# Performance work log

Hardware: AMD Instinct MI355X
Metric: run time of the kernel (lower is better)

The kernel has to match this reference:

```python
import jax, jax.numpy as jnp
import numpy as np

EMBED = 768
HIDDEN = 4 * EMBED
TEMPERATURE = 1.0
LN_EPS = 1e-5


def setup_inputs() -> dict:
    key = jax.random.key(0)
    ks = jax.random.split(key, 10)
    s = 1.0 / np.sqrt(EMBED)
    sh = 1.0 / np.sqrt(HIDDEN)
    return {
        "x": jax.random.normal(ks[0], (32, 577, EMBED), dtype=jnp.float32),
        "Wq": jax.random.normal(ks[1], (EMBED, EMBED), dtype=jnp.float32) * s,
        "Wk": jax.random.normal(ks[2], (EMBED, EMBED), dtype=jnp.float32) * s,
        "Wv": jax.random.normal(ks[3], (EMBED, EMBED), dtype=jnp.float32) * s,
        "ln1_g": jnp.ones((EMBED,), jnp.float32),
        "ln1_b": jnp.zeros((EMBED,), jnp.float32),
        "ln2_g": jnp.ones((EMBED,), jnp.float32),
        "ln2_b": jnp.zeros((EMBED,), jnp.float32),
        "W1": jax.random.normal(ks[4], (EMBED, HIDDEN), dtype=jnp.float32) * s,
        "b1": jnp.zeros((HIDDEN,), jnp.float32),
        "W2": jax.random.normal(ks[5], (HIDDEN, EMBED), dtype=jnp.float32) * sh,
        "b2": jnp.zeros((EMBED,), jnp.float32),
    }


def layer_norm(x, g, b):
    mu = jnp.mean(x, axis=-1, keepdims=True)
    var = jnp.mean(jnp.square(x - mu), axis=-1, keepdims=True)
    return (x - mu) * jax.lax.rsqrt(var + LN_EPS) * g + b


def l2_attention(h, Wq, Wk, Wv):
    # h: [b, s, d]
    Q = h @ Wq
    K = h @ Wk
    V = h @ Wv
    q_sq = jnp.sum(Q * Q, axis=-1, keepdims=True)          # [b, s, 1]
    k_sq = jnp.sum(K * K, axis=-1, keepdims=True)          # [b, s, 1]
    qk = jnp.einsum('bqd,bkd->bqk', Q, K)                  # [b, s, s]
    l2_sq = q_sq + jnp.swapaxes(k_sq, -2, -1) - 2.0 * qk
    attn = jax.nn.softmax(-l2_sq / TEMPERATURE, axis=-1)
    return jnp.einsum('bqk,bkd->bqd', attn, V)


def reference(x, Wq, Wk, Wv, ln1_g, ln1_b, ln2_g, ln2_b, W1, b1, W2, b2):
    x = x + l2_attention(layer_norm(x, ln1_g, ln1_b), Wq, Wk, Wv)
    h = layer_norm(x, ln2_g, ln2_b)
    h = jax.nn.gelu(h @ W1 + b1, approximate=False) @ W2 + b2
    return x + h
```

## Files before the change

kernel.cpp:

```cpp
#include <hip/hip_runtime.h>

#define EMBED 768
#define HIDDEN 3072
#define SEQ 577
#define BATCH 32
#define ROWS (BATCH*SEQ)
#define KPAD 608
#define SLD 640

typedef __attribute__((ext_vector_type(4))) float f32x4;
typedef __attribute__((ext_vector_type(8))) __bf16 bf16x8;
typedef unsigned int __attribute__((address_space(1))) as1_u32;
typedef unsigned int __attribute__((address_space(3))) as3_u32;

__device__ __forceinline__ unsigned short f2b(float f) {
    unsigned int u = __float_as_uint(f);
    u = u + 0x7FFFu + ((u >> 16) & 1u);
    return (unsigned short)(u >> 16);
}
__device__ __forceinline__ float b2f(unsigned short s) {
    return __uint_as_float(((unsigned int)s) << 16);
}
__device__ __forceinline__ void gld16(const unsigned short* g, unsigned short* l) {
    __builtin_amdgcn_global_load_lds((const as1_u32*)g, (as3_u32*)l, 16, 0, 0);
}
__device__ __forceinline__ float gelu_f(float x) {
    float u = x * (0.7978845608028654f + 0.03567740814183f * x * x);
    float e = __expf(2.0f * u);
    float th = 1.0f - 2.0f / (e + 1.0f);
    return 0.5f * x * (1.0f + th);
}

__device__ __forceinline__ int swz_lin() {
    int nx = gridDim.x;
    int lin = blockIdx.y * nx + blockIdx.x;
    if (gridDim.z == 1) {
        int nwg = nx * gridDim.y;
        int q = nwg >> 3, r = nwg & 7;
        int xcd = lin & 7, blk = lin >> 3;
        lin = (xcd < r ? xcd * (q + 1) : r * (q + 1) + (xcd - r) * q) + blk;
    }
    return lin;
}

__global__ void ln_kernel(const float* __restrict__ x, const float* __restrict__ g,
                          const float* __restrict__ b, unsigned short* __restrict__ o) {
    int row = blockIdx.x;
    const float* xr = x + (size_t)row * EMBED;
    int t = threadIdx.x;
    float v0 = xr[t], v1 = xr[t + 256], v2 = xr[t + 512];
    float s = v0 + v1 + v2;
    float ss = v0 * v0 + v1 * v1 + v2 * v2;
#pragma unroll
    for (int d = 32; d; d >>= 1) { s += __shfl_down(s, d); ss += __shfl_down(ss, d); }
    __shared__ float rs[4], rss[4];
    if ((t & 63) == 0) { rs[t >> 6] = s; rss[t >> 6] = ss; }
    __syncthreads();
    s = rs[0] + rs[1] + rs[2] + rs[3];
    ss = rss[0] + rss[1] + rss[2] + rss[3];
    float mu = s * (1.0f / EMBED);
    float var = ss * (1.0f / EMBED) - mu * mu;
    float rstd = rsqrtf(var + 1e-5f);
    unsigned short* orow = o + (size_t)row * EMBED;
    orow[t]       = f2b((v0 - mu) * rstd * g[t]       + b[t]);
    orow[t + 256] = f2b((v1 - mu) * rstd * g[t + 256] + b[t + 256]);
    orow[t + 512] = f2b((v2 - mu) * rstd * g[t + 512] + b[t + 512]);
}

__global__ void ln_split_kernel(const float* __restrict__ x, const float* __restrict__ g,
                                const float* __restrict__ b, unsigned short* __restrict__ oh,
                                unsigned short* __restrict__ ol) {
    int row = blockIdx.x;
    const float* xr = x + (size_t)row * EMBED;
    int t = threadIdx.x;
    float v0 = xr[t], v1 = xr[t + 256], v2 = xr[t + 512];
    float s = v0 + v1 + v2;
    float ss = v0 * v0 + v1 * v1 + v2 * v2;
#pragma unroll
    for (int d = 32; d; d >>= 1) { s += __shfl_down(s, d); ss += __shfl_down(ss, d); }
    __shared__ float rs[4], rss[4];
    if ((t & 63) == 0) { rs[t >> 6] = s; rss[t >> 6] = ss; }
    __syncthreads();
    s = rs[0] + rs[1] + rs[2] + rs[3];
    ss = rss[0] + rss[1] + rss[2] + rss[3];
    float mu = s * (1.0f / EMBED);
    float var = ss * (1.0f / EMBED) - mu * mu;
    float rstd = rsqrtf(var + 1e-5f);
    size_t base = (size_t)row * EMBED;
#pragma unroll
    for (int i = 0; i < 3; i++) {
        int d = t + 256 * i;
        float v = (i == 0 ? v0 : (i == 1 ? v1 : v2));
        float y = (v - mu) * rstd * g[d] + b[d];
        unsigned short h = f2b(y);
        oh[base + d] = h;
        ol[base + d] = f2b(y - b2f(h));
    }
}

__global__ void ksq_kernel(const unsigned short* __restrict__ qh,
                           const unsigned short* __restrict__ ql, float* __restrict__ ksq) {
    int row = blockIdx.x;
    int t = threadIdx.x;
    size_t base = (size_t)row * 1536 + EMBED;
    float s = 0.f;
#pragma unroll
    for (int i = 0; i < 3; i++) {
        int d = t + 256 * i;
        float k = b2f(qh[base + d]) + b2f(ql[base + d]);
        s += k * k;
    }
#pragma unroll
    for (int d = 32; d; d >>= 1) s += __shfl_down(s, d);
    __shared__ float rs[4];
    if ((t & 63) == 0) rs[t >> 6] = s;
    __syncthreads();
    if (t == 0) ksq[row] = rs[0] + rs[1] + rs[2] + rs[3];
}

__global__ void softmax_kernel(const float* __restrict__ S, unsigned short* __restrict__ P) {
    int r = blockIdx.x;
    int t = threadIdx.x;
    const float* sr = S + (size_t)r * SLD;
    float v0 = sr[t];
    float v1 = sr[t + 256];
    float v2 = (t + 512 < SEQ) ? sr[t + 512] : -3.0e38f;
    float m = fmaxf(v0, fmaxf(v1, v2));
#pragma unroll
    for (int d = 32; d; d >>= 1) m = fmaxf(m, __shfl_down(m, d));
    __shared__ float rm[4];
    if ((t & 63) == 0) rm[t >> 6] = m;
    __syncthreads();
    m = fmaxf(fmaxf(rm[0], rm[1]), fmaxf(rm[2], rm[3]));
    float e0 = __expf(v0 - m);
    float e1 = __expf(v1 - m);
    float e2 = (t + 512 < SEQ) ? __expf(v2 - m) : 0.0f;
    float s = e0 + e1 + e2;
#pragma unroll
    for (int d = 32; d; d >>= 1) s += __shfl_down(s, d);
    __shared__ float rsum[4];
    if ((t & 63) == 0) rsum[t >> 6] = s;
    __syncthreads();
    float inv = 1.0f / (rsum[0] + rsum[1] + rsum[2] + rsum[3]);
    unsigned short* pr = P + (size_t)r * KPAD;
    pr[t]       = f2b(e0 * inv);
    pr[t + 256] = f2b(e1 * inv);
    if (t + 512 < KPAD) pr[t + 512] = f2b(e2 * inv);
}

__global__ void wt_kernel(const float* __restrict__ in, unsigned short* __restrict__ out,
                          int K, int N, int outRowOff, int outLd) {
    __shared__ float tile[32][33];
    int n0 = blockIdx.x * 32, k0 = blockIdx.y * 32;
    int tx = threadIdx.x, ty = threadIdx.y;
#pragma unroll
    for (int i = 0; i < 4; i++)
        tile[ty + 8 * i][tx] = in[(size_t)(k0 + ty + 8 * i) * N + (n0 + tx)];
    __syncthreads();
#pragma unroll
    for (int i = 0; i < 4; i++)
        out[(size_t)(outRowOff + n0 + ty + 8 * i) * outLd + (k0 + tx)] = f2b(tile[tx][ty + 8 * i]);
}

__global__ void wt_split2_kernel(const float* __restrict__ Wq, const float* __restrict__ Wk,
                                 unsigned short* __restrict__ oh, unsigned short* __restrict__ ol) {
    const float* in = blockIdx.z ? Wk : Wq;
    int outRowOff = blockIdx.z * EMBED;
    __shared__ float tile[32][33];
    int n0 = blockIdx.x * 32, k0 = blockIdx.y * 32;
    int tx = threadIdx.x, ty = threadIdx.y;
#pragma unroll
    for (int i = 0; i < 4; i++)
        tile[ty + 8 * i][tx] = in[(size_t)(k0 + ty + 8 * i) * EMBED + (n0 + tx)];
    __syncthreads();
#pragma unroll
    for (int i = 0; i < 4; i++) {
        float v = tile[tx][ty + 8 * i];
        unsigned short h = f2b(v);
        size_t idx = (size_t)(outRowOff + n0 + ty + 8 * i) * EMBED + (k0 + tx);
        oh[idx] = h;
        ol[idx] = f2b(v - b2f(h));
    }
}

template <int EPI>
__global__ __launch_bounds__(256, 2) void gemm_bt128(
    const unsigned short* __restrict__ A, int lda, long long sA,
    const unsigned short* __restrict__ B, int ldb, long long sB,
    int M, int N, int K,
    void* __restrict__ C, int ldc, long long sC,
    const float* __restrict__ E, long long sE) {
    __shared__ unsigned short As[2][4096];
    __shared__ unsigned short Bs[2][4096];
    int z = blockIdx.z;
    A += (size_t)z * sA;
    B += (size_t)z * sB;
    int nx = gridDim.x;
    int lin = swz_lin();
    int row0 = (lin / nx) * 128, col0 = (lin % nx) * 128;
    int t = threadIdx.x, l = t & 63, w = t >> 6;
    int wr = w >> 1, wc = w & 1;
    int l15 = l & 15, kb = l >> 4;

    f32x4 acc[4][4] = {};

    int srow = t >> 2;
    int kboff = ((t & 3) ^ ((srow >> 1) & 3)) * 8;

    int aoE[2], boE[2];
#pragma unroll
    for (int c = 0; c < 2; ++c) {
        int ar = row0 + c * 64 + srow; ar = ar < M ? ar : M - 1;
        aoE[c] = ar * lda + kboff;
        int br = col0 + c * 64 + srow; br = br < N ? br : N - 1;
        boE[c] = br * ldb + kboff;
    }
    int aoff[4], boff[4];
#pragma unroll
    for (int m = 0; m < 4; m++) {
        int r = wr * 64 + m * 16 + l15;
        aoff[m] = r * 32 + (kb ^ ((r >> 1) & 3)) * 8;
        int rn = wc * 64 + m * 16 + l15;
        boff[m] = rn * 32 + (kb ^ ((rn >> 1) & 3)) * 8;
    }

    auto compute = [&](int sl) {
        bf16x8 af[4], bfr[4];
#pragma unroll
        for (int m = 0; m < 4; m++) af[m] = *reinterpret_cast<const bf16x8*>(&As[sl][aoff[m]]);
#pragma unroll
        for (int n = 0; n < 4; n++) bfr[n] = *reinterpret_cast<const bf16x8*>(&Bs[sl][boff[n]]);
#pragma unroll
        for (int m = 0; m < 4; m++)
#pragma unroll
            for (int n = 0; n < 4; n++)
                acc[m][n] = __builtin_amdgcn_mfma_f32_16x16x32_bf16(af[m], bfr[n], acc[m][n], 0, 0, 0);
    };

    int ldsoff = t * 8;
    for (int kt = 0; kt < K; kt += 64) {
        gld16(A + (size_t)(aoE[0] + kt), &As[0][ldsoff]);
        gld16(A + (size_t)(aoE[1] + kt), &As[0][2048 + ldsoff]);
        gld16(B + (size_t)(boE[0] + kt), &Bs[0][ldsoff]);
        gld16(B + (size_t)(boE[1] + kt), &Bs[0][2048 + ldsoff]);
        bool has2 = (kt + 32) < K;
        if (has2) {
            gld16(A + (size_t)(aoE[0] + kt + 32), &As[1][ldsoff]);
            gld16(A + (size_t)(aoE[1] + kt + 32), &As[1][2048 + ldsoff]);
            gld16(B + (size_t)(boE[0] + kt + 32), &Bs[1][ldsoff]);
            gld16(B + (size_t)(boE[1] + kt + 32), &Bs[1][2048 + ldsoff]);
        }
        asm volatile("s_waitcnt vmcnt(0)" ::: "memory");
        __builtin_amdgcn_s_barrier();
        __builtin_amdgcn_sched_barrier(0);
        compute(0);
        if (has2) compute(1);
        __builtin_amdgcn_s_barrier();
        __builtin_amdgcn_sched_barrier(0);
    }

    int rbase = row0 + wr * 64 + (l >> 4) * 4;
    int cbase = col0 + wc * 64 + l15;
    auto epi = [&](bool chk) {
#pragma unroll
        for (int m = 0; m < 4; m++) {
#pragma unroll
            for (int n = 0; n < 4; n++) {
                int col = cbase + n * 16;
                if (chk && col >= N) continue;
#pragma unroll
                for (int j = 0; j < 4; j++) {
                    int row = rbase + m * 16 + j;
                    if (chk && row >= M) continue;
                    float v = acc[m][n][j];
                    size_t oidx = (size_t)z * sC + (size_t)row * ldc + col;
                    if (EPI == 0) {
                        ((unsigned short*)C)[oidx] = f2b(v);
                    } else if (EPI == 3) {
                        ((unsigned short*)C)[oidx] = f2b(gelu_f(v + E[col]));
                    } else if (EPI == 4) {
                        ((float*)C)[oidx] += v + E[col];
                    }
                }
            }
        }
    };
    if (row0 + 128 <= M && col0 + 128 <= N) epi(false); else epi(true);
}

template <int EPI>
__global__ __launch_bounds__(512, 4) void gemm_bt256(
    const unsigned short* __restrict__ A, int lda, long long sA,
    const unsigned short* __restrict__ B, int ldb, long long sB,
    int M, int N, int K,
    void* __restrict__ C, int ldc, long long sC,
    const float* __restrict__ E, long long sE) {
    __shared__ unsigned short As[3][8192];
    __shared__ unsigned short Bs[3][4096];
    int z = blockIdx.z;
    A += (size_t)z * sA;
    B += (size_t)z * sB;
    int nx = gridDim.x;
    int lin = swz_lin();
    int row0 = (lin / nx) * 256, col0 = (lin % nx) * 128;
    int t = threadIdx.x, l = t & 63, w = t >> 6;
    int wr = w >> 1, wc = w & 1;
    int l15 = l & 15, kb = l >> 4;

    f32x4 acc[4][4] = {};

    int srow = t >> 2;
    int kboff = ((t & 3) ^ ((srow >> 1) & 3)) * 8;

    int aoE[2], boE;
#pragma unroll
    for (int c = 0; c < 2; ++c) {
        int ar = row0 + c * 128 + srow; ar = ar < M ? ar : M - 1;
        aoE[c] = ar * lda + kboff;
    }
    {
        int br = col0 + srow; br = br < N ? br : N - 1;
        boE = br * ldb + kboff;
    }
    int aoff[4], boff[4];
#pragma unroll
    for (int m = 0; m < 4; m++) {
        int r = wr * 64 + m * 16 + l15;
        aoff[m] = r * 32 + (kb ^ ((r >> 1) & 3)) * 8;
        int rn = wc * 64 + m * 16 + l15;
        boff[m] = rn * 32 + (kb ^ ((rn >> 1) & 3)) * 8;
    }

    auto compute = [&](int sl) {
        bf16x8 af[4], bfr[4];
#pragma unroll
        for (int m = 0; m < 4; m++) af[m] = *reinterpret_cast<const bf16x8*>(&As[sl][aoff[m]]);
#pragma unroll
        for (int n = 0; n < 4; n++) bfr[n] = *reinterpret_cast<const bf16x8*>(&Bs[sl][boff[n]]);
#pragma unroll
        for (int m = 0; m < 4; m++)
#pragma unroll
            for (int n = 0; n < 4; n++)
                acc[m][n] = __builtin_amdgcn_mfma_f32_16x16x32_bf16(af[m], bfr[n], acc[m][n], 0, 0, 0);
    };

    int ldsoff = t * 8;
    for (int kt = 0; kt < K; kt += 96) {
#pragma unroll
        for (int s = 0; s < 3; ++s) {
            int ks = kt + 32 * s;
            if (ks < K) {
                gld16(A + (size_t)(aoE[0] + ks), &As[s][ldsoff]);
                gld16(A + (size_t)(aoE[1] + ks), &As[s][4096 + ldsoff]);
                gld16(B + (size_t)(boE + ks), &Bs[s][ldsoff]);
            }
        }
        asm volatile("s_waitcnt vmcnt(0)" ::: "memory");
        __builtin_amdgcn_s_barrier();
        __builtin_amdgcn_sched_barrier(0);
#pragma unroll
        for (int s = 0; s < 3; ++s)
            if (kt + 32 * s < K) compute(s);
        __builtin_amdgcn_s_barrier();
        __builtin_amdgcn_sched_barrier(0);
    }

    int rbase = row0 + wr * 64 + (l >> 4) * 4;
    int cbase = col0 + wc * 64 + l15;
    auto epi = [&](bool chk) {
#pragma unroll
        for (int m = 0; m < 4; m++) {
#pragma unroll
            for (int n = 0; n < 4; n++) {
                int col = cbase + n * 16;
                if (chk && col >= N) continue;
#pragma unroll
                for (int j = 0; j < 4; j++) {
                    int row = rbase + m * 16 + j;
                    if (chk && row >= M) continue;
                    float v = acc[m][n][j];
                    if (EPI == 5) {
                        int zz = row / SEQ;
                        int cc = row - zz * SEQ;
                        ((unsigned short*)C)[(size_t)zz * (EMBED * KPAD) + (size_t)col * KPAD + cc] = f2b(v);
                    } else {
                        size_t oidx = (size_t)z * sC + (size_t)row * ldc + col;
                        if (EPI == 2) {
                            ((float*)C)[oidx] = E[oidx] + v;
                        } else if (EPI == 4) {
                            ((float*)C)[oidx] += v + E[col];
                        }
                    }
                }
            }
        }
    };
    if (row0 + 256 <= M && col0 + 128 <= N) epi(false); else epi(true);
}

template <int EPI>
__global__ __launch_bounds__(512, 2) void gemm_hp(
    const unsigned short* __restrict__ Ah, const unsigned short* __restrict__ Al, int lda, long long sA,
    const unsigned short* __restrict__ Bh, const unsigned short* __restrict__ Bl, int ldb, long long sB,
    int M, int N, int K,
    void* __restrict__ C, int ldc, long long sC, long long planeOff,
    const float* __restrict__ E, long long sE) {
    __shared__ unsigned short Ash[8192], Asl[8192], Bsh[4096], Bsl[4096];
    int z = blockIdx.z;
    Ah += (size_t)z * sA; Al += (size_t)z * sA;
    Bh += (size_t)z * sB; Bl += (size_t)z * sB;
    int nx = gridDim.x;
    int lin = swz_lin();
    int row0 = (lin / nx) * 256, col0 = (lin % nx) * 128;
    int t = threadIdx.x, l = t & 63, w = t >> 6;
    int wr = w >> 1, wc = w & 1;
    int l15 = l & 15, kb = l >> 4;

    f32x4 acc[4][4] = {};

    int srow = t >> 2;
    int kboff = ((t & 3) ^ ((srow >> 1) & 3)) * 8;

    int aoE[2], boE;
#pragma unroll
    for (int c = 0; c < 2; ++c) {
        int ar = row0 + c * 128 + srow; ar = ar < M ? ar : M - 1;
        aoE[c] = ar * lda + kboff;
    }
    {
        int br = col0 + srow; br = br < N ? br : N - 1;
        boE = br * ldb + kboff;
    }
    int aoff[4], boff[4];
#pragma unroll
    for (int m = 0; m < 4; m++) {
        int r = wr * 64 + m * 16 + l15;
        aoff[m] = r * 32 + (kb ^ ((r >> 1) & 3)) * 8;
        int rn = wc * 64 + m * 16 + l15;
        boff[m] = rn * 32 + (kb ^ ((rn >> 1) & 3)) * 8;
    }

    int ldsoff = t * 8;
    for (int kt = 0; kt < K; kt += 32) {
        gld16(Ah + (size_t)(aoE[0] + kt), &Ash[ldsoff]);
        gld16(Ah + (size_t)(aoE[1] + kt), &Ash[4096 + ldsoff]);
        gld16(Al + (size_t)(aoE[0] + kt), &Asl[ldsoff]);
        gld16(Al + (size_t)(aoE[1] + kt), &Asl[4096 + ldsoff]);
        gld16(Bh + (size_t)(boE + kt), &Bsh[ldsoff]);
        gld16(Bl + (size_t)(boE + kt), &Bsl[ldsoff]);
        __syncthreads();
        bf16x8 afh[4], afl[4], bfh[4], bfl[4];
#pragma unroll
        for (int m = 0; m < 4; m++) {
            afh[m] = *reinterpret_cast<const bf16x8*>(&Ash[aoff[m]]);
            afl[m] = *reinterpret_cast<const bf16x8*>(&Asl[aoff[m]]);
        }
#pragma unroll
        for (int n = 0; n < 4; n++) {
            bfh[n] = *reinterpret_cast<const bf16x8*>(&Bsh[boff[n]]);
            bfl[n] = *reinterpret_cast<const bf16x8*>(&Bsl[boff[n]]);
        }
#pragma unroll
        for (int m = 0; m < 4; m++)
#pragma unroll
            for (int n = 0; n < 4; n++) {
                acc[m][n] = __builtin_amdgcn_mfma_f32_16x16x32_bf16(afh[m], bfh[n], acc[m][n], 0, 0, 0);
                acc[m][n] = __builtin_amdgcn_mfma_f32_16x16x32_bf16(afh[m], bfl[n], acc[m][n], 0, 0, 0);
                acc[m][n] = __builtin_amdgcn_mfma_f32_16x16x32_bf16(afl[m], bfh[n], acc[m][n], 0, 0, 0);
            }
        __syncthreads();
    }

    int rbase = row0 + wr * 64 + (l >> 4) * 4;
    int cbase = col0 + wc * 64 + l15;
    auto epi = [&](bool chk) {
#pragma unroll
        for (int m = 0; m < 4; m++) {
#pragma unroll
            for (int n = 0; n < 4; n++) {
                int col = cbase + n * 16;
                if (chk && col >= N) continue;
#pragma unroll
                for (int j = 0; j < 4; j++) {
                    int row = rbase + m * 16 + j;
                    if (chk && row >= M) continue;
                    float v = acc[m][n][j];
                    size_t oidx = (size_t)z * sC + (size_t)row * ldc + col;
                    if (EPI == 0) {
                        unsigned short h = f2b(v);
                        ((unsigned short*)C)[oidx] = h;
                        ((unsigned short*)C)[oidx + planeOff] = f2b(v - b2f(h));
                    } else if (EPI == 1) {
                        ((float*)C)[oidx] = 2.0f * v - E[(size_t)z * sE + col];
                    }
                }
            }
        }
    };
    if (row0 + 256 <= M && col0 + 128 <= N) epi(false); else epi(true);
}

extern "C" void kernel_launch(void* const* d_in, const int* in_sizes, int n_in,
                              void* d_out, int out_size, void* d_ws, size_t ws_size,
                              hipStream_t stream) {
    const float* x   = (const float*)d_in[0];
    const float* Wq  = (const float*)d_in[1];
    const float* Wk  = (const float*)d_in[2];
    const float* Wv  = (const float*)d_in[3];
    const float* g1  = (const float*)d_in[4];
    const float* be1 = (const float*)d_in[5];
    const float* g2  = (const float*)d_in[6];
    const float* be2 = (const float*)d_in[7];
    const float* W1  = (const float*)d_in[8];
    const float* bb1 = (const float*)d_in[9];
    const float* W2  = (const float*)d_in[10];
    const float* bb2 = (const float*)d_in[11];
    float* out = (float*)d_out;

    char* ws = (char*)d_ws;
    size_t off = 0;
    auto alloc = [&](size_t bytes) -> char* {
        char* p = ws + off;
        off += (bytes + 255) & ~(size_t)255;
        return p;
    };
    unsigned short* wqkTh = (unsigned short*)alloc((size_t)1536 * EMBED * 2);
    unsigned short* wqkTl = (unsigned short*)alloc((size_t)1536 * EMBED * 2);
    unsigned short* wvT   = (unsigned short*)alloc((size_t)EMBED * EMBED * 2);
    unsigned short* w1T   = (unsigned short*)alloc((size_t)HIDDEN * EMBED * 2);
    unsigned short* w2T   = (unsigned short*)alloc((size_t)EMBED * HIDDEN * 2);
    float*          ksqb  = (float*)alloc((size_t)ROWS * 4);
    char* regB = alloc((size_t)ROWS * HIDDEN * 2);
    char* regC = alloc((size_t)2 * ROWS * EMBED * 2);
    unsigned short* vtb   = (unsigned short*)alloc((size_t)BATCH * EMBED * KPAD * 2);
    unsigned short* Pbuf  = (unsigned short*)alloc((size_t)ROWS * KPAD * 2);
    if (off > ws_size) return;

    unsigned short* qkh  = (unsigned short*)regB;
    unsigned short* qkl  = qkh + (size_t)ROWS * 1536;
    unsigned short* hid  = (unsigned short*)regB;
    unsigned short* h1h  = (unsigned short*)regC;
    unsigned short* h1l  = h1h + (size_t)ROWS * EMBED;
    float*          Sbuf = (float*)regC;
    unsigned short* h2   = (unsigned short*)regC;

    dim3 b256(256), b512(512), bT(32, 8);

    wt_split2_kernel<<<dim3(24, 24, 2), bT, 0, stream>>>(Wq, Wk, wqkTh, wqkTl);
    wt_kernel<<<dim3(24, 24), bT, 0, stream>>>(Wv, wvT, EMBED, EMBED, 0, EMBED);
    wt_kernel<<<dim3(96, 24), bT, 0, stream>>>(W1, w1T, EMBED, HIDDEN, 0, EMBED);
    wt_kernel<<<dim3(24, 96), bT, 0, stream>>>(W2, w2T, HIDDEN, EMBED, 0, HIDDEN);

    ln_split_kernel<<<ROWS, b256, 0, stream>>>(x, g1, be1, h1h, h1l);

    gemm_hp<0><<<dim3(12, 73, 1), b512, 0, stream>>>(
        h1h, h1l, EMBED, 0, wqkTh, wqkTl, EMBED, 0,
        ROWS, 1536, EMBED, qkh, 1536, 0, (long long)ROWS * 1536, nullptr, 0);

    gemm_bt256<5><<<dim3(6, 73, 1), b512, 0, stream>>>(
        h1h, EMBED, 0, wvT, EMBED, 0, ROWS, EMBED, EMBED, vtb, 0, 0, nullptr, 0);

    ksq_kernel<<<ROWS, b256, 0, stream>>>(qkh, qkl, ksqb);

    gemm_hp<1><<<dim3(5, 3, 32), b512, 0, stream>>>(
        qkh, qkl, 1536, (long long)SEQ * 1536, qkh + EMBED, qkl + EMBED, 1536, (long long)SEQ * 1536,
        SEQ, SEQ, EMBED, Sbuf, SLD, (long long)SEQ * SLD, 0, ksqb, SEQ);

    softmax_kernel<<<ROWS, b256, 0, stream>>>(Sbuf, Pbuf);

    gemm_bt256<2><<<dim3(6, 3, 32), b512, 0, stream>>>(
        Pbuf, KPAD, (long long)SEQ * KPAD, vtb, KPAD, (long long)EMBED * KPAD,
        SEQ, EMBED, KPAD, out, EMBED, (long long)SEQ * EMBED, x, (long long)SEQ * EMBED);

    ln_kernel<<<ROWS, b256, 0, stream>>>(out, g2, be2, h2);

    gemm_bt128<3><<<dim3(24, 145, 1), b256, 0, stream>>>(
        h2, EMBED, 0, w1T, EMBED, 0, ROWS, HIDDEN, EMBED, hid, HIDDEN, 0, bb1, 0);

    gemm_bt256<4><<<dim3(6, 73, 1), b512, 0, stream>>>(
        hid, HIDDEN, 0, w2T, HIDDEN, 0, ROWS, EMBED, HIDDEN, out, EMBED, 0, bb2, 0);
}
```

Before: 727.6 us.

## Fuse V projection into split-precision QK GEMM launch with per-tile single-pass mode

The separate bf16 GEMM that produced the transposed V buffer is removed. The QK split-precision GEMM launch is widened to cover Q, K and V columns using one concatenated transposed weight. Tiles whose columns fall in the V range skip the low-precision loads and extra MFMAs, and write bf16 transposed V directly. This saves a kernel launch and a pass over the LN output. In exchange, V now goes through the 256x128 hp tile path with a runtime branch inside the k-loop.

```diff
diff --git a/kernel.cpp b/kernel.cpp
--- a/kernel.cpp
+++ b/kernel.cpp
@@ -379,17 +379,11 @@
                     int row = rbase + m * 16 + j;
                     if (chk && row >= M) continue;
                     float v = acc[m][n][j];
-                    if (EPI == 5) {
-                        int zz = row / SEQ;
-                        int cc = row - zz * SEQ;
-                        ((unsigned short*)C)[(size_t)zz * (EMBED * KPAD) + (size_t)col * KPAD + cc] = f2b(v);
-                    } else {
-                        size_t oidx = (size_t)z * sC + (size_t)row * ldc + col;
-                        if (EPI == 2) {
-                            ((float*)C)[oidx] = E[oidx] + v;
-                        } else if (EPI == 4) {
-                            ((float*)C)[oidx] += v + E[col];
-                        }
+                    size_t oidx = (size_t)z * sC + (size_t)row * ldc + col;
+                    if (EPI == 2) {
+                        ((float*)C)[oidx] = E[oidx] + v;
+                    } else if (EPI == 4) {
+                        ((float*)C)[oidx] += v + E[col];
                     }
                 }
             }
@@ -404,7 +398,8 @@
     const unsigned short* __restrict__ Bh, const unsigned short* __restrict__ Bl, int ldb, long long sB,
     int M, int N, int K,
     void* __restrict__ C, int ldc, long long sC, long long planeOff,
-    const float* __restrict__ E, long long sE) {
+    const float* __restrict__ E, long long sE,
+    int vcol0, unsigned short* __restrict__ vt) {
     __shared__ unsigned short Ash[8192], Asl[8192], Bsh[4096], Bsl[4096];
     int z = blockIdx.z;
     Ah += (size_t)z * sA; Al += (size_t)z * sA;
@@ -412,6 +407,7 @@
     int nx = gridDim.x;
     int lin = swz_lin();
     int row0 = (lin / nx) * 256, col0 = (lin % nx) * 128;
+    bool vpass = (EPI == 0) && (col0 >= vcol0);
     int t = threadIdx.x, l = t & 63, w = t >> 6;
     int wr = w >> 1, wc = w & 1;
     int l15 = l & 15, kb = l >> 4;
@@ -444,30 +440,37 @@
     for (int kt = 0; kt < K; kt += 32) {
         gld16(Ah + (size_t)(aoE[0] + kt), &Ash[ldsoff]);
         gld16(Ah + (size_t)(aoE[1] + kt), &Ash[4096 + ldsoff]);
-        gld16(Al + (size_t)(aoE[0] + kt), &Asl[ldsoff]);
-        gld16(Al + (size_t)(aoE[1] + kt), &Asl[4096 + ldsoff]);
         gld16(Bh + (size_t)(boE + kt), &Bsh[ldsoff]);
-        gld16(Bl + (size_t)(boE + kt), &Bsl[ldsoff]);
+        if (!vpass) {
+            gld16(Al + (size_t)(aoE[0] + kt), &Asl[ldsoff]);
+            gld16(Al + (size_t)(aoE[1] + kt), &Asl[4096 + ldsoff]);
+            gld16(Bl + (size_t)(boE + kt), &Bsl[ldsoff]);
+        }
         __syncthreads();
-        bf16x8 afh[4], afl[4], bfh[4], bfl[4];
-#pragma unroll
-        for (int m = 0; m < 4; m++) {
-            afh[m] = *reinterpret_cast<const bf16x8*>(&Ash[aoff[m]]);
-            afl[m] = *reinterpret_cast<const bf16x8*>(&Asl[aoff[m]]);
-        }
-#pragma unroll
-        for (int n = 0; n < 4; n++) {
-            bfh[n] = *reinterpret_cast<const bf16x8*>(&Bsh[boff[n]]);
-            bfl[n] = *reinterpret_cast<const bf16x8*>(&Bsl[boff[n]]);
-        }
+        bf16x8 afh[4], bfh[4];
+#pragma unroll
+        for (int m = 0; m < 4; m++) afh[m] = *reinterpret_cast<const bf16x8*>(&Ash[aoff[m]]);
+#pragma unroll
+        for (int n = 0; n < 4; n++) bfh[n] = *reinterpret_cast<const bf16x8*>(&Bsh[boff[n]]);
 #pragma unroll
         for (int m = 0; m < 4; m++)
 #pragma unroll
-            for (int n = 0; n < 4; n++) {
+            for (int n = 0; n < 4; n++)
                 acc[m][n] = __builtin_amdgcn_mfma_f32_16x16x32_bf16(afh[m], bfh[n], acc[m][n], 0, 0, 0);
-                acc[m][n] = __builtin_amdgcn_mfma_f32_16x16x32_bf16(afh[m], bfl[n], acc[m][n], 0, 0, 0);
-                acc[m][n] = __builtin_amdgcn_mfma_f32_16x16x32_bf16(afl[m], bfh[n], acc[m][n], 0, 0, 0);
-            }
+        if (!vpass) {
+            bf16x8 afl[4], bfl[4];
+#pragma unroll
+            for (int m = 0; m < 4; m++) afl[m] = *reinterpret_cast<const bf16x8*>(&Asl[aoff[m]]);
+#pragma unroll
+            for (int n = 0; n < 4; n++) bfl[n] = *reinterpret_cast<const bf16x8*>(&Bsl[boff[n]]);
+#pragma unroll
+            for (int m = 0; m < 4; m++)
+#pragma unroll
+                for (int n = 0; n < 4; n++) {
+                    acc[m][n] = __builtin_amdgcn_mfma_f32_16x16x32_bf16(afh[m], bfl[n], acc[m][n], 0, 0, 0);
+                    acc[m][n] = __builtin_amdgcn_mfma_f32_16x16x32_bf16(afl[m], bfh[n], acc[m][n], 0, 0, 0);
+                }
+        }
         __syncthreads();
     }
 
@@ -485,13 +488,19 @@
                     int row = rbase + m * 16 + j;
                     if (chk && row >= M) continue;
                     float v = acc[m][n][j];
-                    size_t oidx = (size_t)z * sC + (size_t)row * ldc + col;
-                    if (EPI == 0) {
-                        unsigned short h = f2b(v);
-                        ((unsigned short*)C)[oidx] = h;
-                        ((unsigned short*)C)[oidx + planeOff] = f2b(v - b2f(h));
-                    } else if (EPI == 1) {
-                        ((float*)C)[oidx] = 2.0f * v - E[(size_t)z * sE + col];
+                    if (vpass) {
+                        int zz = row / SEQ;
+                        int cc = row - zz * SEQ;
+                        vt[(size_t)zz * (EMBED * KPAD) + (size_t)(col - vcol0) * KPAD + cc] = f2b(v);
+                    } else {
+                        size_t oidx = (size_t)z * sC + (size_t)row * ldc + col;
+                        if (EPI == 0) {
+                            unsigned short h = f2b(v);
+                            ((unsigned short*)C)[oidx] = h;
+                            ((unsigned short*)C)[oidx + planeOff] = f2b(v - b2f(h));
+                        } else if (EPI == 1) {
+                            ((float*)C)[oidx] = 2.0f * v - E[(size_t)z * sE + col];
+                        }
                     }
                 }
             }
@@ -524,9 +533,8 @@
         off += (bytes + 255) & ~(size_t)255;
         return p;
     };
-    unsigned short* wqkTh = (unsigned short*)alloc((size_t)1536 * EMBED * 2);
-    unsigned short* wqkTl = (unsigned short*)alloc((size_t)1536 * EMBED * 2);
-    unsigned short* wvT   = (unsigned short*)alloc((size_t)EMBED * EMBED * 2);
+    unsigned short* wqkvTh = (unsigned short*)alloc((size_t)2304 * EMBED * 2);
+    unsigned short* wqkvTl = (unsigned short*)alloc((size_t)2304 * EMBED * 2);
     unsigned short* w1T   = (unsigned short*)alloc((size_t)HIDDEN * EMBED * 2);
     unsigned short* w2T   = (unsigned short*)alloc((size_t)EMBED * HIDDEN * 2);
     float*          ksqb  = (float*)alloc((size_t)ROWS * 4);
@@ -546,25 +554,24 @@
 
     dim3 b256(256), b512(512), bT(32, 8);
 
-    wt_split2_kernel<<<dim3(24, 24, 2), bT, 0, stream>>>(Wq, Wk, wqkTh, wqkTl);
-    wt_kernel<<<dim3(24, 24), bT, 0, stream>>>(Wv, wvT, EMBED, EMBED, 0, EMBED);
+    wt_split2_kernel<<<dim3(24, 24, 2), bT, 0, stream>>>(Wq, Wk, wqkvTh, wqkvTl);
+    wt_kernel<<<dim3(24, 24), bT, 0, stream>>>(Wv, wqkvTh, EMBED, EMBED, 1536, EMBED);
     wt_kernel<<<dim3(96, 24), bT, 0, stream>>>(W1, w1T, EMBED, HIDDEN, 0, EMBED);
     wt_kernel<<<dim3(24, 96), bT, 0, stream>>>(W2, w2T, HIDDEN, EMBED, 0, HIDDEN);
 
     ln_split_kernel<<<ROWS, b256, 0, stream>>>(x, g1, be1, h1h, h1l);
 
-    gemm_hp<0><<<dim3(12, 73, 1), b512, 0, stream>>>(
-        h1h, h1l, EMBED, 0, wqkTh, wqkTl, EMBED, 0,
-        ROWS, 1536, EMBED, qkh, 1536, 0, (long long)ROWS * 1536, nullptr, 0);
-
-    gemm_bt256<5><<<dim3(6, 73, 1), b512, 0, stream>>>(
-        h1h, EMBED, 0, wvT, EMBED, 0, ROWS, EMBED, EMBED, vtb, 0, 0, nullptr, 0);
+    gemm_hp<0><<<dim3(18, 73, 1), b512, 0, stream>>>(
+        h1h, h1l, EMBED, 0, wqkvTh, wqkvTl, EMBED, 0,
+        ROWS, 2304, EMBED, qkh, 1536, 0, (long long)ROWS * 1536, nullptr, 0,
+        1536, vtb);
 
     ksq_kernel<<<ROWS, b256, 0, stream>>>(qkh, qkl, ksqb);
 
     gemm_hp<1><<<dim3(5, 3, 32), b512, 0, stream>>>(
         qkh, qkl, 1536, (long long)SEQ * 1536, qkh + EMBED, qkl + EMBED, 1536, (long long)SEQ * 1536,
-        SEQ, SEQ, EMBED, Sbuf, SLD, (long long)SEQ * SLD, 0, ksqb, SEQ);
+        SEQ, SEQ, EMBED, Sbuf, SLD, (long long)SEQ * SLD, 0, ksqb, SEQ,
+        1 << 30, nullptr);
 
     softmax_kernel<<<ROWS, b256, 0, stream>>>(Sbuf, Pbuf);
 
```

New measurement: 782.9 us. 7.6% more time.
